# Kernel tuning notes

Hardware: AMD Instinct MI355X
Metric: run time of the kernel (lower is better)

## Reference

```python
import jax, jax.numpy as jnp
import numpy as np

NUM_NODES = 50000


def setup_inputs() -> dict:
    key = jax.random.key(0)
    ks = jax.random.split(key, 5)
    d = 128
    E = 600000
    x = jax.random.normal(ks[0], (NUM_NODES, d), dtype=jnp.float32)
    edge_attr = jax.random.normal(ks[1], (E, d), dtype=jnp.float32)
    receivers_idx = jax.random.randint(ks[2], (E,), 0, NUM_NODES)
    # MLP params: Linear(2d -> d), ReLU, Linear(d -> d). Stored as [in, out].
    W1 = jax.random.normal(ks[3], (2 * d, d), dtype=jnp.float32) / np.sqrt(2 * d)
    b1 = jnp.zeros((d,), dtype=jnp.float32)
    W2 = jax.random.normal(ks[4], (d, d), dtype=jnp.float32) / np.sqrt(d)
    b2 = jnp.zeros((d,), dtype=jnp.float32)
    return {"x": x, "edge_attr": edge_attr, "receivers_idx": receivers_idx,
            "W1": W1, "b1": b1, "W2": W2, "b2": b2}


def reference(x, edge_attr, receivers_idx, W1, b1, W2, b2):
    # scatter_add(edge_attr, receivers_idx, dim=0, dim_size=num_nodes)
    agg = jax.ops.segment_sum(edge_attr, receivers_idx, num_segments=NUM_NODES)  # [N, d]
    collected = jnp.concatenate([x, agg], axis=-1)  # [N, 2d]
    h = jax.nn.relu(collected @ W1 + b1)  # [N, d]
    out = h @ W2 + b2                     # [N, d]
    # Original returns Data(x=out, edge_attr=edge_attr, edge_index=edge_index);
    # edge_attr/edge_index pass through unchanged, so return the new node features.
    return out
```

## Files before the change

kernel.cpp:

```cpp
#include <hip/hip_runtime.h>
#include <hip/hip_bf16.h>

#define N_NODES 50000
#define DIM 128
#define N_EDGES 600000
#define MAX_DEG 64

typedef __attribute__((ext_vector_type(8))) short short8;
typedef __attribute__((ext_vector_type(4))) float f32x4;

__device__ __forceinline__ unsigned short f2bf_u(float f) {
    return __bfloat16_as_ushort(__float2bfloat16(f));
}

__global__ __launch_bounds__(256) void fill_direct(
    const int* __restrict__ ridx, int* __restrict__ cnt, int* __restrict__ elist) {
    int e = blockIdx.x * 256 + threadIdx.x;
    if (e < N_EDGES) {
        int node = ridx[e];
        int pos = atomicAdd(&cnt[node], 1);
        if (pos < MAX_DEG) elist[(size_t)node * MAX_DEG + pos] = e;
    }
}

__global__ __launch_bounds__(256) void prep_kernel(
    const float* __restrict__ W1,
    const float* __restrict__ W2,
    const float* __restrict__ x,
    __hip_bfloat16* __restrict__ W1t,
    __hip_bfloat16* __restrict__ W2t,
    __hip_bfloat16* __restrict__ xa) {
    int b = blockIdx.x;
    if (b < 192) {
        int t = b * 256 + threadIdx.x;
        if (t < 256 * 128) {
            int k = t >> 7, n = t & 127;
            W1t[n * 256 + k] = __float2bfloat16(W1[t]);
        } else {
            int q = t - 256 * 128;
            int k = q >> 7, n = q & 127;
            W2t[n * 128 + k] = __float2bfloat16(W2[q]);
        }
    } else {
        int t = (b - 192) * 256 + threadIdx.x;
        int node = t >> 5;
        int c = t & 31;
        if (node < N_NODES) {
            f32x4 v = *reinterpret_cast<const f32x4*>(x + (size_t)node * DIM + c * 4);
            ushort2 p0 = { f2bf_u(v[0]), f2bf_u(v[1]) };
            ushort2 p1 = { f2bf_u(v[2]), f2bf_u(v[3]) };
            uint2 packed = { *(unsigned*)&p0, *(unsigned*)&p1 };
            *reinterpret_cast<uint2*>(xa + (size_t)node * 256 + c * 4) = packed;
        }
    }
}

__global__ __launch_bounds__(256) void aggregate_kernel(
    const float* __restrict__ edge_attr,
    const int* __restrict__ elist,
    const int* __restrict__ cnt,
    __hip_bfloat16* __restrict__ xa) {
    const int node = blockIdx.x * 4 + (threadIdx.x >> 6);
    const int lane = threadIdx.x & 63;
    if (node >= N_NODES) return;
    int deg = cnt[node];
    deg = deg < MAX_DEG ? deg : MAX_DEG;
    const int* el = elist + (size_t)node * MAX_DEG;
    float sx = 0.f, sy = 0.f;
    int i = 0;
    for (; i + 4 <= deg; i += 4) {
        int e0 = el[i], e1 = el[i + 1], e2 = el[i + 2], e3 = el[i + 3];
        float2 v0 = *reinterpret_cast<const float2*>(edge_attr + (size_t)e0 * DIM + lane * 2);
        float2 v1 = *reinterpret_cast<const float2*>(edge_attr + (size_t)e1 * DIM + lane * 2);
        float2 v2 = *reinterpret_cast<const float2*>(edge_attr + (size_t)e2 * DIM + lane * 2);
        float2 v3 = *reinterpret_cast<const float2*>(edge_attr + (size_t)e3 * DIM + lane * 2);
        sx += (v0.x + v1.x) + (v2.x + v3.x);
        sy += (v0.y + v1.y) + (v2.y + v3.y);
    }
    for (; i < deg; i++) {
        int e0 = el[i];
        float2 v0 = *reinterpret_cast<const float2*>(edge_attr + (size_t)e0 * DIM + lane * 2);
        sx += v0.x;
        sy += v0.y;
    }
    unsigned packed = ((unsigned)f2bf_u(sy) << 16) | (unsigned)f2bf_u(sx);
    *reinterpret_cast<unsigned*>(xa + (size_t)node * 256 + 128 + lane * 2) = packed;
}

__global__ __launch_bounds__(256) void mlp_kernel(
    const __hip_bfloat16* __restrict__ xa,
    const __hip_bfloat16* __restrict__ W1t,
    const float* __restrict__ b1,
    const __hip_bfloat16* __restrict__ W2t,
    const float* __restrict__ b2,
    float* __restrict__ out) {
    __shared__ __hip_bfloat16 sH[128][136];

    const int wave = threadIdx.x >> 6;
    const int lane = threadIdx.x & 63;
    const int quad = lane >> 4;
    const int l16  = lane & 15;
    const int rowBase = blockIdx.x * 128 + wave * 32;

    f32x4 accH[2][8] = {};
#pragma unroll
    for (int ks = 0; ks < 8; ks++) {
        const int k0 = ks * 32 + quad * 8;
        short8 a[2];
#pragma unroll
        for (int rt = 0; rt < 2; rt++) {
            int row = rowBase + rt * 16 + l16;
            row = row < N_NODES ? row : N_NODES - 1;
            a[rt] = *reinterpret_cast<const short8*>(xa + (size_t)row * 256 + k0);
        }
#pragma unroll
        for (int nt = 0; nt < 8; nt++) {
            short8 b = *reinterpret_cast<const short8*>(W1t + (nt * 16 + l16) * 256 + k0);
            accH[0][nt] = __builtin_amdgcn_mfma_f32_16x16x32_bf16(a[0], b, accH[0][nt], 0, 0, 0);
            accH[1][nt] = __builtin_amdgcn_mfma_f32_16x16x32_bf16(a[1], b, accH[1][nt], 0, 0, 0);
        }
    }

#pragma unroll
    for (int nt = 0; nt < 8; nt++) {
        const float bias = b1[nt * 16 + l16];
#pragma unroll
        for (int rt = 0; rt < 2; rt++) {
#pragma unroll
            for (int i = 0; i < 4; i++) {
                float v = accH[rt][nt][i] + bias;
                v = v > 0.0f ? v : 0.0f;
                int r = wave * 32 + rt * 16 + quad * 4 + i;
                sH[r][nt * 16 + l16] = __float2bfloat16(v);
            }
        }
    }
    __syncthreads();

    f32x4 accO[2][8] = {};
#pragma unroll
    for (int ks = 0; ks < 4; ks++) {
        const int k0 = ks * 32 + quad * 8;
        short8 a[2];
#pragma unroll
        for (int rt = 0; rt < 2; rt++) {
            int r = wave * 32 + rt * 16 + l16;
            a[rt] = *reinterpret_cast<const short8*>(&sH[r][k0]);
        }
#pragma unroll
        for (int nt = 0; nt < 8; nt++) {
            short8 b = *reinterpret_cast<const short8*>(W2t + (nt * 16 + l16) * 128 + k0);
            accO[0][nt] = __builtin_amdgcn_mfma_f32_16x16x32_bf16(a[0], b, accO[0][nt], 0, 0, 0);
            accO[1][nt] = __builtin_amdgcn_mfma_f32_16x16x32_bf16(a[1], b, accO[1][nt], 0, 0, 0);
        }
    }

#pragma unroll
    for (int nt = 0; nt < 8; nt++) {
        const float bias = b2[nt * 16 + l16];
#pragma unroll
        for (int rt = 0; rt < 2; rt++) {
#pragma unroll
            for (int i = 0; i < 4; i++) {
                int row = rowBase + rt * 16 + quad * 4 + i;
                if (row < N_NODES) {
                    out[(size_t)row * DIM + nt * 16 + l16] = accO[rt][nt][i] + bias;
                }
            }
        }
    }
}

extern "C" void kernel_launch(void* const* d_in, const int* in_sizes, int n_in,
                              void* d_out, int out_size, void* d_ws, size_t ws_size,
                              hipStream_t stream) {
    const float* x         = (const float*)d_in[0];
    const float* edge_attr = (const float*)d_in[1];
    const int*   ridx      = (const int*)d_in[2];
    const float* W1        = (const float*)d_in[3];
    const float* b1        = (const float*)d_in[4];
    const float* W2        = (const float*)d_in[5];
    const float* b2        = (const float*)d_in[6];
    float* out = (float*)d_out;

    char* w = (char*)d_ws;
    int* elist = (int*)w;                     w += (size_t)N_NODES * MAX_DEG * 4;
    int* cnt   = (int*)w;                     w += (size_t)N_NODES * 4;
    __hip_bfloat16* xa  = (__hip_bfloat16*)w; w += (size_t)N_NODES * 256 * 2;
    __hip_bfloat16* W1t = (__hip_bfloat16*)w; w += 256 * 128 * 2;
    __hip_bfloat16* W2t = (__hip_bfloat16*)w;

    hipMemsetAsync(cnt, 0, (size_t)N_NODES * 4, stream);
    fill_direct<<<dim3((N_EDGES + 255) / 256), dim3(256), 0, stream>>>(ridx, cnt, elist);
    prep_kernel<<<dim3(192 + (N_NODES * 32 + 255) / 256), dim3(256), 0, stream>>>(
        W1, W2, x, W1t, W2t, xa);
    aggregate_kernel<<<dim3((N_NODES + 3) / 4), dim3(256), 0, stream>>>(edge_attr, elist, cnt, xa);
    mlp_kernel<<<dim3((N_NODES + 127) / 128), dim3(256), 0, stream>>>(xa, W1t, b1, W2t, b2, out);
}
```

Baseline: 539.4 us.

## Fuse aggregation, x conversion and MLP into one kernel; merge fill and prep

Aggregation of edge features now happens inside the MLP kernel, with each wave summing its 32 nodes and writing bf16 results straight into shared memory instead of a global xa buffer. x is read as fp32 and converted to bf16 inline in the first GEMM. Edge-index loads are vectorised with int4 and the loop is unrolled to 8. The edge-list fill and weight transpose are merged into a single launch. This removes the xa round trip through global memory and two launches, but the fused kernel has only about 391 blocks, so there is far less parallelism for hiding gather latency than the old per-node aggregate kernel had.

Measured after the change: 563.0 us. 4.4% more time.

```diff
diff --git a/kernel.cpp b/kernel.cpp
--- a/kernel.cpp
+++ b/kernel.cpp
@@ -13,26 +13,23 @@
     return __bfloat16_as_ushort(__float2bfloat16(f));
 }
 
-__global__ __launch_bounds__(256) void fill_direct(
-    const int* __restrict__ ridx, int* __restrict__ cnt, int* __restrict__ elist) {
-    int e = blockIdx.x * 256 + threadIdx.x;
-    if (e < N_EDGES) {
-        int node = ridx[e];
-        int pos = atomicAdd(&cnt[node], 1);
-        if (pos < MAX_DEG) elist[(size_t)node * MAX_DEG + pos] = e;
-    }
-}
-
-__global__ __launch_bounds__(256) void prep_kernel(
-    const float* __restrict__ W1,
-    const float* __restrict__ W2,
-    const float* __restrict__ x,
-    __hip_bfloat16* __restrict__ W1t,
-    __hip_bfloat16* __restrict__ W2t,
-    __hip_bfloat16* __restrict__ xa) {
+#define FILL_BLOCKS ((N_EDGES + 255) / 256)
+#define PREP_BLOCKS 192
+
+__global__ __launch_bounds__(256) void fill_prep(
+    const int* __restrict__ ridx, int* __restrict__ cnt, int* __restrict__ elist,
+    const float* __restrict__ W1, const float* __restrict__ W2,
+    __hip_bfloat16* __restrict__ W1t, __hip_bfloat16* __restrict__ W2t) {
     int b = blockIdx.x;
-    if (b < 192) {
-        int t = b * 256 + threadIdx.x;
+    if (b < FILL_BLOCKS) {
+        int e = b * 256 + threadIdx.x;
+        if (e < N_EDGES) {
+            int node = ridx[e];
+            int pos = atomicAdd(&cnt[node], 1);
+            if (pos < MAX_DEG) elist[(size_t)node * MAX_DEG + pos] = e;
+        }
+    } else {
+        int t = (b - FILL_BLOCKS) * 256 + threadIdx.x;
         if (t < 256 * 128) {
             int k = t >> 7, n = t & 127;
             W1t[n * 256 + k] = __float2bfloat16(W1[t]);
@@ -41,60 +38,20 @@
             int k = q >> 7, n = q & 127;
             W2t[n * 128 + k] = __float2bfloat16(W2[q]);
         }
-    } else {
-        int t = (b - 192) * 256 + threadIdx.x;
-        int node = t >> 5;
-        int c = t & 31;
-        if (node < N_NODES) {
-            f32x4 v = *reinterpret_cast<const f32x4*>(x + (size_t)node * DIM + c * 4);
-            ushort2 p0 = { f2bf_u(v[0]), f2bf_u(v[1]) };
-            ushort2 p1 = { f2bf_u(v[2]), f2bf_u(v[3]) };
-            uint2 packed = { *(unsigned*)&p0, *(unsigned*)&p1 };
-            *reinterpret_cast<uint2*>(xa + (size_t)node * 256 + c * 4) = packed;
-        }
-    }
-}
-
-__global__ __launch_bounds__(256) void aggregate_kernel(
+    }
+}
+
+__global__ __launch_bounds__(256) void fused_kernel(
+    const float* __restrict__ x,
     const float* __restrict__ edge_attr,
     const int* __restrict__ elist,
     const int* __restrict__ cnt,
-    __hip_bfloat16* __restrict__ xa) {
-    const int node = blockIdx.x * 4 + (threadIdx.x >> 6);
-    const int lane = threadIdx.x & 63;
-    if (node >= N_NODES) return;
-    int deg = cnt[node];
-    deg = deg < MAX_DEG ? deg : MAX_DEG;
-    const int* el = elist + (size_t)node * MAX_DEG;
-    float sx = 0.f, sy = 0.f;
-    int i = 0;
-    for (; i + 4 <= deg; i += 4) {
-        int e0 = el[i], e1 = el[i + 1], e2 = el[i + 2], e3 = el[i + 3];
-        float2 v0 = *reinterpret_cast<const float2*>(edge_attr + (size_t)e0 * DIM + lane * 2);
-        float2 v1 = *reinterpret_cast<const float2*>(edge_attr + (size_t)e1 * DIM + lane * 2);
-        float2 v2 = *reinterpret_cast<const float2*>(edge_attr + (size_t)e2 * DIM + lane * 2);
-        float2 v3 = *reinterpret_cast<const float2*>(edge_attr + (size_t)e3 * DIM + lane * 2);
-        sx += (v0.x + v1.x) + (v2.x + v3.x);
-        sy += (v0.y + v1.y) + (v2.y + v3.y);
-    }
-    for (; i < deg; i++) {
-        int e0 = el[i];
-        float2 v0 = *reinterpret_cast<const float2*>(edge_attr + (size_t)e0 * DIM + lane * 2);
-        sx += v0.x;
-        sy += v0.y;
-    }
-    unsigned packed = ((unsigned)f2bf_u(sy) << 16) | (unsigned)f2bf_u(sx);
-    *reinterpret_cast<unsigned*>(xa + (size_t)node * 256 + 128 + lane * 2) = packed;
-}
-
-__global__ __launch_bounds__(256) void mlp_kernel(
-    const __hip_bfloat16* __restrict__ xa,
     const __hip_bfloat16* __restrict__ W1t,
     const float* __restrict__ b1,
     const __hip_bfloat16* __restrict__ W2t,
     const float* __restrict__ b2,
     float* __restrict__ out) {
-    __shared__ __hip_bfloat16 sH[128][136];
+    __shared__ __hip_bfloat16 sBuf[128][136];
 
     const int wave = threadIdx.x >> 6;
     const int lane = threadIdx.x & 63;
@@ -102,16 +59,75 @@
     const int l16  = lane & 15;
     const int rowBase = blockIdx.x * 128 + wave * 32;
 
+    for (int i = 0; i < 32; i++) {
+        const int node = rowBase + i;
+        unsigned packed = 0u;
+        if (node < N_NODES) {
+            int deg = cnt[node];
+            deg = deg < MAX_DEG ? deg : MAX_DEG;
+            const int* el = elist + (size_t)node * MAX_DEG;
+            float sx = 0.f, sy = 0.f;
+            int j = 0;
+            for (; j + 8 <= deg; j += 8) {
+                int4 ea = *reinterpret_cast<const int4*>(el + j);
+                int4 eb = *reinterpret_cast<const int4*>(el + j + 4);
+                float2 v0 = *reinterpret_cast<const float2*>(edge_attr + (size_t)ea.x * DIM + lane * 2);
+                float2 v1 = *reinterpret_cast<const float2*>(edge_attr + (size_t)ea.y * DIM + lane * 2);
+                float2 v2 = *reinterpret_cast<const float2*>(edge_attr + (size_t)ea.z * DIM + lane * 2);
+                float2 v3 = *reinterpret_cast<const float2*>(edge_attr + (size_t)ea.w * DIM + lane * 2);
+                float2 v4 = *reinterpret_cast<const float2*>(edge_attr + (size_t)eb.x * DIM + lane * 2);
+                float2 v5 = *reinterpret_cast<const float2*>(edge_attr + (size_t)eb.y * DIM + lane * 2);
+                float2 v6 = *reinterpret_cast<const float2*>(edge_attr + (size_t)eb.z * DIM + lane * 2);
+                float2 v7 = *reinterpret_cast<const float2*>(edge_attr + (size_t)eb.w * DIM + lane * 2);
+                sx += ((v0.x + v1.x) + (v2.x + v3.x)) + ((v4.x + v5.x) + (v6.x + v7.x));
+                sy += ((v0.y + v1.y) + (v2.y + v3.y)) + ((v4.y + v5.y) + (v6.y + v7.y));
+            }
+            if (j + 4 <= deg) {
+                int4 ea = *reinterpret_cast<const int4*>(el + j);
+                float2 v0 = *reinterpret_cast<const float2*>(edge_attr + (size_t)ea.x * DIM + lane * 2);
+                float2 v1 = *reinterpret_cast<const float2*>(edge_attr + (size_t)ea.y * DIM + lane * 2);
+                float2 v2 = *reinterpret_cast<const float2*>(edge_attr + (size_t)ea.z * DIM + lane * 2);
+                float2 v3 = *reinterpret_cast<const float2*>(edge_attr + (size_t)ea.w * DIM + lane * 2);
+                sx += (v0.x + v1.x) + (v2.x + v3.x);
+                sy += (v0.y + v1.y) + (v2.y + v3.y);
+                j += 4;
+            }
+            for (; j < deg; j++) {
+                int e0 = el[j];
+                float2 v0 = *reinterpret_cast<const float2*>(edge_attr + (size_t)e0 * DIM + lane * 2);
+                sx += v0.x;
+                sy += v0.y;
+            }
+            packed = ((unsigned)f2bf_u(sy) << 16) | (unsigned)f2bf_u(sx);
+        }
+        *reinterpret_cast<unsigned*>(&sBuf[wave * 32 + i][lane * 2]) = packed;
+    }
+
     f32x4 accH[2][8] = {};
 #pragma unroll
     for (int ks = 0; ks < 8; ks++) {
         const int k0 = ks * 32 + quad * 8;
         short8 a[2];
-#pragma unroll
-        for (int rt = 0; rt < 2; rt++) {
-            int row = rowBase + rt * 16 + l16;
-            row = row < N_NODES ? row : N_NODES - 1;
-            a[rt] = *reinterpret_cast<const short8*>(xa + (size_t)row * 256 + k0);
+        if (ks < 4) {
+#pragma unroll
+            for (int rt = 0; rt < 2; rt++) {
+                int row = rowBase + rt * 16 + l16;
+                row = row < N_NODES ? row : N_NODES - 1;
+                const float* xp = x + (size_t)row * DIM + k0;
+                f32x4 u = *reinterpret_cast<const f32x4*>(xp);
+                f32x4 v = *reinterpret_cast<const f32x4*>(xp + 4);
+                short8 av = { (short)f2bf_u(u[0]), (short)f2bf_u(u[1]),
+                              (short)f2bf_u(u[2]), (short)f2bf_u(u[3]),
+                              (short)f2bf_u(v[0]), (short)f2bf_u(v[1]),
+                              (short)f2bf_u(v[2]), (short)f2bf_u(v[3]) };
+                a[rt] = av;
+            }
+        } else {
+#pragma unroll
+            for (int rt = 0; rt < 2; rt++) {
+                int r = wave * 32 + rt * 16 + l16;
+                a[rt] = *reinterpret_cast<const short8*>(&sBuf[r][k0 - 128]);
+            }
         }
 #pragma unroll
         for (int nt = 0; nt < 8; nt++) {
@@ -131,11 +147,10 @@
                 float v = accH[rt][nt][i] + bias;
                 v = v > 0.0f ? v : 0.0f;
                 int r = wave * 32 + rt * 16 + quad * 4 + i;
-                sH[r][nt * 16 + l16] = __float2bfloat16(v);
-            }
-        }
-    }
-    __syncthreads();
+                sBuf[r][nt * 16 + l16] = __float2bfloat16(v);
+            }
+        }
+    }
 
     f32x4 accO[2][8] = {};
 #pragma unroll
@@ -145,7 +160,7 @@
 #pragma unroll
         for (int rt = 0; rt < 2; rt++) {
             int r = wave * 32 + rt * 16 + l16;
-            a[rt] = *reinterpret_cast<const short8*>(&sH[r][k0]);
+            a[rt] = *reinterpret_cast<const short8*>(&sBuf[r][k0]);
         }
 #pragma unroll
         for (int nt = 0; nt < 8; nt++) {
@@ -186,14 +201,12 @@
     char* w = (char*)d_ws;
     int* elist = (int*)w;                     w += (size_t)N_NODES * MAX_DEG * 4;
     int* cnt   = (int*)w;                     w += (size_t)N_NODES * 4;
-    __hip_bfloat16* xa  = (__hip_bfloat16*)w; w += (size_t)N_NODES * 256 * 2;
     __hip_bfloat16* W1t = (__hip_bfloat16*)w; w += 256 * 128 * 2;
     __hip_bfloat16* W2t = (__hip_bfloat16*)w;
 
     hipMemsetAsync(cnt, 0, (size_t)N_NODES * 4, stream);
-    fill_direct<<<dim3((N_EDGES + 255) / 256), dim3(256), 0, stream>>>(ridx, cnt, elist);
-    prep_kernel<<<dim3(192 + (N_NODES * 32 + 255) / 256), dim3(256), 0, stream>>>(
-        W1, W2, x, W1t, W2t, xa);
-    aggregate_kernel<<<dim3((N_NODES + 3) / 4), dim3(256), 0, stream>>>(edge_attr, elist, cnt, xa);
-    mlp_kernel<<<dim3((N_NODES + 127) / 128), dim3(256), 0, stream>>>(xa, W1t, b1, W2t, b2, out);
-}
+    fill_prep<<<dim3(FILL_BLOCKS + PREP_BLOCKS), dim3(256), 0, stream>>>(
+        ridx, cnt, elist, W1, W2, W1t, W2t);
+    fused_kernel<<<dim3((N_NODES + 127) / 128), dim3(256), 0, stream>>>(
+        x, edge_attr, elist, cnt, W1t, b1, W2t, b2, out);
+}
```
